# Optimization experiments

Measured on AMD Instinct MI355X. Metric: run time of the kernel, lower is better.

## Reference

```python
import jax, jax.numpy as jnp
import numpy as np

DIM = 768
FF = 3072
E = 8          # num_experts
K = 2          # top_k
H = 12         # n_heads
HD = DIM // H  # head dim
LN_EPS = 1e-5


def _layernorm(x, g, b):
    m = jnp.mean(x, axis=-1, keepdims=True)
    v = jnp.var(x, axis=-1, keepdims=True)
    return (x - m) * jax.lax.rsqrt(v + LN_EPS) * g + b


def _attention(x, Wqkv, Wproj):
    B, T, D = x.shape
    qkv = (x @ Wqkv).reshape(B, T, 3, H, HD)
    q, k, v = qkv[:, :, 0], qkv[:, :, 1], qkv[:, :, 2]  # [B,T,H,HD]
    scores = jnp.einsum('bqhd,bkhd->bhqk', q, k) * jnp.float32(HD) ** -0.5
    attn = jax.nn.softmax(scores, axis=-1)  # non-causal SDPA
    out = jnp.einsum('bhqk,bkhd->bqhd', attn, v).reshape(B, T, D)
    return out @ Wproj


def _moe(x, Wrouter, W1, W2):
    # world_size == 1 path of MoEFeedForward.forward:
    # gate_and_sort -> per-expert FFN -> weighted index_add unpermute.
    # Equivalent math: out[t] = sum_k softmax(topk_logits)[t,k] * expert_{idx[t,k]}(x[t]).
    B, T, D = x.shape
    xf = x.reshape(-1, D)                       # [N, D]
    N = xf.shape[0]
    logits = xf @ Wrouter                        # [N, E]
    topk_w, topk_idx = jax.lax.top_k(logits, K)  # [N, K]
    topk_w = jax.nn.softmax(topk_w.astype(jnp.float32), axis=-1).astype(x.dtype)
    # Combined per-expert weight for each token (sums duplicates, 0 if unrouted).
    we = jnp.zeros((N, E), x.dtype).at[jnp.arange(N)[:, None], topk_idx].add(topk_w)  # [N, E]

    def body(acc, expert):
        W1e, W2e, we_e = expert                 # [D,FF], [FF,D], [N]
        h = jax.nn.gelu(xf @ W1e, approximate=False)  # exact GELU like nn.GELU()
        return acc + we_e[:, None] * (h @ W2e), None

    out, _ = jax.lax.scan(body, jnp.zeros_like(xf), (W1, W2, we.T))
    return out.reshape(B, T, D)


def setup_inputs() -> dict:
    key = jax.random.key(0)
    ks = jax.random.split(key, 7)
    B, T = 4, 1024
    init = lambda k, shape, fan: jax.random.normal(k, shape, jnp.float32) * (fan ** -0.5)
    return {
        'x': jax.random.normal(ks[0], (B, T, DIM), jnp.float32),
        'Wqkv': init(ks[1], (DIM, 3 * DIM), DIM),
        'Wproj': init(ks[2], (DIM, DIM), DIM),
        'Wrouter': init(ks[3], (DIM, E), DIM),
        'W1': init(ks[4], (E, DIM, FF), DIM),
        'W2': init(ks[5], (E, FF, DIM), FF),
        'ln1_g': jnp.ones((DIM,), jnp.float32), 'ln1_b': jnp.zeros((DIM,), jnp.float32),
        'ln2_g': jnp.ones((DIM,), jnp.float32), 'ln2_b': jnp.zeros((DIM,), jnp.float32),
    }


def reference(x, Wqkv, Wproj, Wrouter, W1, W2, ln1_g, ln1_b, ln2_g, ln2_b):
    # PipelinedMoEBlock: pre-LN attention + pre-LN MoE FFN, residual connections.
    x = x + _attention(_layernorm(x, ln1_g, ln1_b), Wqkv, Wproj)
    x = x + _moe(_layernorm(x, ln2_g, ln2_b), Wrouter, W1, W2)
    return x
```

## Files before the change

### kernel.cpp

```cpp
#include <hip/hip_runtime.h>
#include <math.h>

typedef unsigned short u16;
typedef __attribute__((ext_vector_type(8))) short short8;
typedef __attribute__((ext_vector_type(4))) float f32x4;

#define DIMC   768
#define TOK    4096
#define NQKVC  2304
#define FFC    3072
#define NEXP   8
#define NHEAD  12
#define HDIM   64
#define SEQ    1024
#define NBATCH 4
#define SLOTS  9216

__device__ __forceinline__ float bf2f(u16 v) {
    unsigned int u = ((unsigned int)v) << 16;
    float f; __builtin_memcpy(&f, &u, 4); return f;
}
__device__ __forceinline__ u16 f2bf(float f) {
    unsigned int u; __builtin_memcpy(&u, &f, 4);
    u = (u + 0x7fffu + ((u >> 16) & 1u)) >> 16;
    return (u16)u;
}

__device__ __forceinline__ float fast_gelu(float v) {
    float x = fabsf(v) * 0.70710678118654752f;
    float t = __builtin_amdgcn_rcpf(1.f + 0.3275911f * x);
    float y = t * (0.254829592f + t * (-0.284496736f + t * (1.421413741f +
              t * (-1.453152027f + t * 1.061405429f))));
    float er = 1.f - y * __expf(-x * x);
    er = (v < 0.f) ? -er : er;
    return 0.5f * v * (1.f + er);
}

__device__ __forceinline__ void async16(u16* lds, const u16* gp) {
    __builtin_amdgcn_global_load_lds(
        (const __attribute__((address_space(1))) unsigned int*)gp,
        (__attribute__((address_space(3))) unsigned int*)lds, 16, 0, 0);
}

__global__ __launch_bounds__(256) void ln_split_kernel(const float* __restrict__ x,
                                                       const float* __restrict__ g,
                                                       const float* __restrict__ b,
                                                       u16* __restrict__ yh,
                                                       u16* __restrict__ yl) {
    int row = blockIdx.x, tid = threadIdx.x;
    const float* xr = x + (size_t)row * DIMC;
    float v[3];
#pragma unroll
    for (int i = 0; i < 3; i++) v[i] = xr[tid + 256 * i];
    float s = v[0] + v[1] + v[2];
    float q = v[0]*v[0] + v[1]*v[1] + v[2]*v[2];
#pragma unroll
    for (int o = 32; o; o >>= 1) { s += __shfl_down(s, o, 64); q += __shfl_down(q, o, 64); }
    __shared__ float rs[4], rq[4];
    if ((tid & 63) == 0) { rs[tid >> 6] = s; rq[tid >> 6] = q; }
    __syncthreads();
    s = rs[0] + rs[1] + rs[2] + rs[3];
    q = rq[0] + rq[1] + rq[2] + rq[3];
    float mean = s * (1.f / DIMC);
    float var  = q * (1.f / DIMC) - mean * mean;
    float rstd = rsqrtf(var + 1e-5f);
#pragma unroll
    for (int i = 0; i < 3; i++) {
        int c = tid + 256 * i;
        float o = (v[i] - mean) * rstd * g[c] + b[c];
        u16 h = f2bf(o);
        yh[(size_t)row * DIMC + c] = h;
        yl[(size_t)row * DIMC + c] = f2bf(o - bf2f(h));
    }
}

__global__ __launch_bounds__(256) void ln_bf_kernel(const float* __restrict__ x,
                                                    const float* __restrict__ g,
                                                    const float* __restrict__ b,
                                                    u16* __restrict__ yb,
                                                    float* __restrict__ yf) {
    int row = blockIdx.x, tid = threadIdx.x;
    const float* xr = x + (size_t)row * DIMC;
    float v[3];
#pragma unroll
    for (int i = 0; i < 3; i++) v[i] = xr[tid + 256 * i];
    float s = v[0] + v[1] + v[2];
    float q = v[0]*v[0] + v[1]*v[1] + v[2]*v[2];
#pragma unroll
    for (int o = 32; o; o >>= 1) { s += __shfl_down(s, o, 64); q += __shfl_down(q, o, 64); }
    __shared__ float rs[4], rq[4];
    if ((tid & 63) == 0) { rs[tid >> 6] = s; rq[tid >> 6] = q; }
    __syncthreads();
    s = rs[0] + rs[1] + rs[2] + rs[3];
    q = rq[0] + rq[1] + rq[2] + rq[3];
    float mean = s * (1.f / DIMC);
    float var  = q * (1.f / DIMC) - mean * mean;
    float rstd = rsqrtf(var + 1e-5f);
#pragma unroll
    for (int i = 0; i < 3; i++) {
        int c = tid + 256 * i;
        float o = (v[i] - mean) * rstd * g[c] + b[c];
        yb[(size_t)row * DIMC + c] = f2bf(o);
        yf[(size_t)row * DIMC + c] = o;
    }
}

__global__ __launch_bounds__(256) void split_hl_kernel(const float* __restrict__ src,
                                                       u16* __restrict__ dh,
                                                       u16* __restrict__ dl) {
    size_t i = ((size_t)blockIdx.x * 256 + threadIdx.x) * 4;
#pragma unroll
    for (int k = 0; k < 4; k++) {
        float v = src[i + k];
        u16 h = f2bf(v);
        dh[i + k] = h;
        dl[i + k] = f2bf(v - bf2f(h));
    }
}

__global__ __launch_bounds__(256) void transpose_split_kernel(
    const float* __restrict__ src, u16* __restrict__ dh, u16* __restrict__ dl,
    int s_rs, int d_rs, long s_bs, long d_bs) {
    __shared__ u16 th[32][33], tl[32][33];
    int z = blockIdx.z;
    const float* sb = src + (long)z * s_bs;
    int r0 = blockIdx.y * 32, c0 = blockIdx.x * 32;
    int tx = threadIdx.x & 31, ty = threadIdx.x >> 5;
#pragma unroll
    for (int i = 0; i < 4; i++) {
        float v = sb[(size_t)(r0 + ty + 8 * i) * s_rs + c0 + tx];
        u16 h = f2bf(v);
        th[ty + 8 * i][tx] = h;
        tl[ty + 8 * i][tx] = f2bf(v - bf2f(h));
    }
    __syncthreads();
#pragma unroll
    for (int i = 0; i < 4; i++) {
        size_t o = (long)z * d_bs + (size_t)(c0 + ty + 8 * i) * d_rs + r0 + tx;
        dh[o] = th[tx][ty + 8 * i];
        dl[o] = tl[tx][ty + 8 * i];
    }
}

__global__ __launch_bounds__(256) void transpose_f2b_kernel(
    const float* __restrict__ src, u16* __restrict__ dst,
    int s_rs, int d_rs, long s_bs, long d_bs) {
    __shared__ u16 tile[32][33];
    int z = blockIdx.z;
    const float* sb = src + (long)z * s_bs;
    int r0 = blockIdx.y * 32, c0 = blockIdx.x * 32;
    int tx = threadIdx.x & 31, ty = threadIdx.x >> 5;
#pragma unroll
    for (int i = 0; i < 4; i++)
        tile[ty + 8 * i][tx] = f2bf(sb[(size_t)(r0 + ty + 8 * i) * s_rs + c0 + tx]);
    __syncthreads();
#pragma unroll
    for (int i = 0; i < 4; i++)
        dst[(long)z * d_bs + (size_t)(c0 + ty + 8 * i) * d_rs + r0 + tx] = tile[tx][ty + 8 * i];
}

__global__ __launch_bounds__(256) void transpose_b2b_kernel(
    const u16* __restrict__ src, u16* __restrict__ dst,
    int s_rs, int d_rs, long s_bs1, int s_n1, long s_bs2, long d_bs) {
    __shared__ u16 tile[32][33];
    int z = blockIdx.z;
    const u16* sb = src + (long)(z / s_n1) * s_bs1 + (long)(z % s_n1) * s_bs2;
    u16* db = dst + (long)z * d_bs;
    int r0 = blockIdx.y * 32, c0 = blockIdx.x * 32;
    int tx = threadIdx.x & 31, ty = threadIdx.x >> 5;
#pragma unroll
    for (int i = 0; i < 4; i++)
        tile[ty + 8 * i][tx] = sb[(size_t)(r0 + ty + 8 * i) * s_rs + c0 + tx];
    __syncthreads();
#pragma unroll
    for (int i = 0; i < 4; i++)
        db[(size_t)(c0 + ty + 8 * i) * d_rs + r0 + tx] = tile[tx][ty + 8 * i];
}

template<int EPI, int OUT>
__global__ __launch_bounds__(256)
void gemm3_kernel(const u16* __restrict__ Ah, const u16* __restrict__ Al, int lda, long aBS,
                  const u16* __restrict__ Bh, const u16* __restrict__ Bl, int ldb, long bBS,
                  void* __restrict__ C0, void* __restrict__ C1, int ldc, long cBS,
                  int M, int N, int K, float alpha, const float* __restrict__ R) {
    __shared__ u16 Ash[128 * 32], Asl[128 * 32], Bsh[128 * 32], Bsl[128 * 32];
    int bm = blockIdx.y, bn = blockIdx.x, bz = blockIdx.z;
    int m0 = bm * 128, n0 = bn * 128;
    const u16* Ahb = Ah + (long)bz * aBS;
    const u16* Alb = Al + (long)bz * aBS;
    const u16* Bhb = Bh + (long)bz * bBS;
    const u16* Blb = Bl + (long)bz * bBS;
    int tid = threadIdx.x, wv = tid >> 6, ln = tid & 63;
    int quad = ln >> 4, l15 = ln & 15;
    int wm = wv & 1, wn = wv >> 1;
    f32x4 acc[4][4];
#pragma unroll
    for (int i = 0; i < 4; i++)
#pragma unroll
        for (int j = 0; j < 4; j++) acc[i][j] = (f32x4)0.f;
    int srow = ln >> 2, schk = (ln & 3) * 8;

    for (int k0 = 0; k0 < K; k0 += 32) {
#pragma unroll
        for (int j = 0; j < 2; j++) {
            int r = 32 * wv + 16 * j + srow;
            size_t ao = (size_t)(m0 + r) * lda + k0 + schk;
            async16(&Ash[(32 * wv + 16 * j) * 32], Ahb + ao);
            async16(&Asl[(32 * wv + 16 * j) * 32], Alb + ao);
            size_t bo = (size_t)(n0 + r) * ldb + k0 + schk;
            async16(&Bsh[(32 * wv + 16 * j) * 32], Bhb + bo);
            async16(&Bsl[(32 * wv + 16 * j) * 32], Blb + bo);
        }
        __syncthreads();
        short8 ah[4], al4[4], bh[4], bl4[4];
#pragma unroll
        for (int mi = 0; mi < 4; mi++) {
            int off = (64 * wm + 16 * mi + l15) * 32 + quad * 8;
            ah[mi]  = *(const short8*)&Ash[off];
            al4[mi] = *(const short8*)&Asl[off];
        }
#pragma unroll
        for (int ni = 0; ni < 4; ni++) {
            int off = (64 * wn + 16 * ni + l15) * 32 + quad * 8;
            bh[ni]  = *(const short8*)&Bsh[off];
            bl4[ni] = *(const short8*)&Bsl[off];
        }
#pragma unroll
        for (int mi = 0; mi < 4; mi++)
#pragma unroll
            for (int ni = 0; ni < 4; ni++) {
                acc[mi][ni] = __builtin_amdgcn_mfma_f32_16x16x32_bf16(ah[mi],  bh[ni],  acc[mi][ni], 0, 0, 0);
                acc[mi][ni] = __builtin_amdgcn_mfma_f32_16x16x32_bf16(ah[mi],  bl4[ni], acc[mi][ni], 0, 0, 0);
                acc[mi][ni] = __builtin_amdgcn_mfma_f32_16x16x32_bf16(al4[mi], bh[ni],  acc[mi][ni], 0, 0, 0);
            }
        __syncthreads();
    }
#pragma unroll
    for (int mi = 0; mi < 4; mi++) {
#pragma unroll
        for (int r = 0; r < 4; r++) {
            int row = m0 + 64 * wm + 16 * mi + quad * 4 + r;
#pragma unroll
            for (int ni = 0; ni < 4; ni++) {
                int col = n0 + 64 * wn + 16 * ni + l15;
                size_t idx = (long)bz * cBS + (size_t)row * ldc + col;
                float v = acc[mi][ni][r] * alpha;
                if (EPI == 3) v += R[idx];
                if (OUT == 1) ((float*)C0)[idx] = v;
                else {
                    u16 h = f2bf(v);
                    ((u16*)C0)[idx] = h;
                    ((u16*)C1)[idx] = f2bf(v - bf2f(h));
                }
            }
        }
    }
}

__global__ __launch_bounds__(256)
void gemm3_pv_kernel(const u16* __restrict__ Ph,
                     const u16* __restrict__ VTh_, const u16* __restrict__ VTl_,
                     float* __restrict__ attf, int b) {
    __shared__ u16 Ash[64 * 32], Asl[64 * 32], Bsh[64 * 32], Bsl[64 * 32];
    int kz = blockIdx.x, qt = blockIdx.y, h = blockIdx.z;
    int tid = threadIdx.x, wv = tid >> 6, ln = tid & 63;
    int quad = ln >> 4, l15 = ln & 15;
    const u16* Ah = Ph + (size_t)h * SEQ * 2 * SEQ;
    const u16* Al = Ah + SEQ;
    const u16* Bh = VTh_ + (size_t)h * HDIM * SEQ;
    const u16* Bl = VTl_ + (size_t)h * HDIM * SEQ;
    int m0 = qt * 64;
    f32x4 acc[4];
#pragma unroll
    for (int i = 0; i < 4; i++) acc[i] = (f32x4)0.f;
    int srow = ln >> 2, schk = (ln & 3) * 8;
    int kbase = kz * (SEQ / 4);
    for (int k0 = kbase; k0 < kbase + SEQ / 4; k0 += 32) {
        int r = 16 * wv + srow;
        async16(&Ash[(16 * wv) * 32], Ah + (size_t)(m0 + r) * 2 * SEQ + k0 + schk);
        async16(&Asl[(16 * wv) * 32], Al + (size_t)(m0 + r) * 2 * SEQ + k0 + schk);
        async16(&Bsh[(16 * wv) * 32], Bh + (size_t)r * SEQ + k0 + schk);
        async16(&Bsl[(16 * wv) * 32], Bl + (size_t)r * SEQ + k0 + schk);
        __syncthreads();
        short8 a_h = *(const short8*)&Ash[(16 * wv + l15) * 32 + quad * 8];
        short8 a_l = *(const short8*)&Asl[(16 * wv + l15) * 32 + quad * 8];
#pragma unroll
        for (int ni = 0; ni < 4; ni++) {
            short8 b_h = *(const short8*)&Bsh[(16 * ni + l15) * 32 + quad * 8];
            short8 b_l = *(const short8*)&Bsl[(16 * ni + l15) * 32 + quad * 8];
            acc[ni] = __builtin_amdgcn_mfma_f32_16x16x32_bf16(a_h, b_h, acc[ni], 0, 0, 0);
            acc[ni] = __builtin_amdgcn_mfma_f32_16x16x32_bf16(a_h, b_l, acc[ni], 0, 0, 0);
            acc[ni] = __builtin_amdgcn_mfma_f32_16x16x32_bf16(a_l, b_h, acc[ni], 0, 0, 0);
        }
        __syncthreads();
    }
#pragma unroll
    for (int ni = 0; ni < 4; ni++)
#pragma unroll
        for (int r = 0; r < 4; r++) {
            int q = m0 + 16 * wv + quad * 4 + r;
            int d = h * HDIM + 16 * ni + l15;
            atomicAdd(&attf[((size_t)b * SEQ + q) * DIMC + d], acc[ni][r]);
        }
}

template<int EPI, int OUTF>
__global__ __launch_bounds__(256)
void gemm_moe_kernel(const u16* __restrict__ A, int lda,
                     const u16* __restrict__ B, int ldb,
                     void* __restrict__ Cv, int ldc,
                     int N, int K,
                     const int* __restrict__ seg, long expStride) {
    __shared__ u16 As[128 * 32];
    __shared__ u16 Bs[128 * 32];
    int m0 = blockIdx.y * 128, n0 = blockIdx.x * 128;
    if (m0 >= seg[8]) return;
    int e = 0;
#pragma unroll
    for (int i = 1; i < 8; i++) if (m0 >= seg[i]) e = i;
    const u16* Bp = B + (long)e * expStride;
    int tid = threadIdx.x, wv = tid >> 6, ln = tid & 63;
    int quad = ln >> 4, l15 = ln & 15;
    int wm = wv & 1, wn = wv >> 1;
    f32x4 acc[4][4];
#pragma unroll
    for (int i = 0; i < 4; i++)
#pragma unroll
        for (int j = 0; j < 4; j++) acc[i][j] = (f32x4)0.f;
    int srow = ln >> 2, schk = (ln & 3) * 8;
    for (int k0 = 0; k0 < K; k0 += 32) {
#pragma unroll
        for (int j = 0; j < 2; j++) {
            int r = 32 * wv + 16 * j + srow;
            async16(&As[(32 * wv + 16 * j) * 32], A + (size_t)(m0 + r) * lda + k0 + schk);
            async16(&Bs[(32 * wv + 16 * j) * 32], Bp + (size_t)(n0 + r) * ldb + k0 + schk);
        }
        __syncthreads();
        short8 af[4], bfr[4];
#pragma unroll
        for (int mi = 0; mi < 4; mi++)
            af[mi] = *(const short8*)&As[(64 * wm + 16 * mi + l15) * 32 + quad * 8];
#pragma unroll
        for (int ni = 0; ni < 4; ni++)
            bfr[ni] = *(const short8*)&Bs[(64 * wn + 16 * ni + l15) * 32 + quad * 8];
#pragma unroll
        for (int mi = 0; mi < 4; mi++)
#pragma unroll
            for (int ni = 0; ni < 4; ni++)
                acc[mi][ni] = __builtin_amdgcn_mfma_f32_16x16x32_bf16(af[mi], bfr[ni], acc[mi][ni], 0, 0, 0);
        __syncthreads();
    }
#pragma unroll
    for (int mi = 0; mi < 4; mi++) {
#pragma unroll
        for (int r = 0; r < 4; r++) {
            int row = m0 + 64 * wm + 16 * mi + quad * 4 + r;
#pragma unroll
            for (int ni = 0; ni < 4; ni++) {
                int col = n0 + 64 * wn + 16 * ni + l15;
                float v = acc[mi][ni][r];
                if (EPI == 2) v = fast_gelu(v);
                size_t idx = (size_t)row * ldc + col;
                if (OUTF) ((float*)Cv)[idx] = v;
                else      ((u16*)Cv)[idx] = f2bf(v);
            }
        }
    }
}

__global__ __launch_bounds__(256)
void gemm_moe_n64_kernel(const u16* __restrict__ A, int lda,
                         const u16* __restrict__ B, int ldb,
                         float* __restrict__ C, int ldc,
                         int K, const int* __restrict__ seg, long expStride) {
    __shared__ u16 As[128 * 32];
    __shared__ u16 Bs[64 * 32];
    int m0 = blockIdx.y * 128, n0 = blockIdx.x * 64;
    if (m0 >= seg[8]) return;
    int e = 0;
#pragma unroll
    for (int i = 1; i < 8; i++) if (m0 >= seg[i]) e = i;
    const u16* Bp = B + (long)e * expStride;
    int tid = threadIdx.x, wv = tid >> 6, ln = tid & 63;
    int quad = ln >> 4, l15 = ln & 15;
    f32x4 acc[2][4];
#pragma unroll
    for (int i = 0; i < 2; i++)
#pragma unroll
        for (int j = 0; j < 4; j++) acc[i][j] = (f32x4)0.f;
    int srow = ln >> 2, schk = (ln & 3) * 8;
    for (int k0 = 0; k0 < K; k0 += 32) {
#pragma unroll
        for (int j = 0; j < 2; j++) {
            int r = 32 * wv + 16 * j + srow;
            async16(&As[(32 * wv + 16 * j) * 32], A + (size_t)(m0 + r) * lda + k0 + schk);
        }
        {
            int r = 16 * wv + srow;
            async16(&Bs[(16 * wv) * 32], Bp + (size_t)(n0 + r) * ldb + k0 + schk);
        }
        __syncthreads();
        short8 af[2], bfr[4];
#pragma unroll
        for (int mi = 0; mi < 2; mi++)
            af[mi] = *(const short8*)&As[(32 * wv + 16 * mi + l15) * 32 + quad * 8];
#pragma unroll
        for (int ni = 0; ni < 4; ni++)
            bfr[ni] = *(const short8*)&Bs[(16 * ni + l15) * 32 + quad * 8];
#pragma unroll
        for (int mi = 0; mi < 2; mi++)
#pragma unroll
            for (int ni = 0; ni < 4; ni++)
                acc[mi][ni] = __builtin_amdgcn_mfma_f32_16x16x32_bf16(af[mi], bfr[ni], acc[mi][ni], 0, 0, 0);
        __syncthreads();
    }
#pragma unroll
    for (int mi = 0; mi < 2; mi++)
#pragma unroll
        for (int r = 0; r < 4; r++) {
            int row = m0 + 32 * wv + 16 * mi + quad * 4 + r;
#pragma unroll
            for (int ni = 0; ni < 4; ni++) {
                int col = n0 + 16 * ni + l15;
                C[(size_t)row * ldc + col] = acc[mi][ni][r];
            }
        }
}

__global__ __launch_bounds__(256) void softmax_split_kernel(float* __restrict__ S) {
    size_t row = blockIdx.x;
    float* p = S + row * (size_t)SEQ;
    u16* ph = (u16*)p;
    u16* pl = (u16*)p + SEQ;
    int tid = threadIdx.x;
    float v[4];
#pragma unroll
    for (int i = 0; i < 4; i++) v[i] = p[tid + 256 * i];
    float m = fmaxf(fmaxf(v[0], v[1]), fmaxf(v[2], v[3]));
#pragma unroll
    for (int o = 32; o; o >>= 1) m = fmaxf(m, __shfl_down(m, o, 64));
    __shared__ float red[4], red2[4];
    if ((tid & 63) == 0) red[tid >> 6] = m;
    __syncthreads();
    m = fmaxf(fmaxf(red[0], red[1]), fmaxf(red[2], red[3]));
    float e[4], s = 0.f;
#pragma unroll
    for (int i = 0; i < 4; i++) { e[i] = expf(v[i] - m); s += e[i]; }
#pragma unroll
    for (int o = 32; o; o >>= 1) s += __shfl_down(s, o, 64);
    if ((tid & 63) == 0) red2[tid >> 6] = s;
    __syncthreads();
    s = red2[0] + red2[1] + red2[2] + red2[3];
    float inv = 1.f / s;
#pragma unroll
    for (int i = 0; i < 4; i++) {
        int c = tid + 256 * i;
        float w = e[i] * inv;
        u16 h = f2bf(w);
        ph[c] = h;
        pl[c] = f2bf(w - bf2f(h));
    }
}

__global__ __launch_bounds__(256) void router_kernel(const float* __restrict__ h2f,
                                                     const float* __restrict__ Wr,
                                                     int* __restrict__ topk_idx,
                                                     float* __restrict__ topk_w,
                                                     int* __restrict__ counts) {
    int t = blockIdx.x, tid = threadIdx.x;
    __shared__ float part[256 * 8];
    float l[8];
#pragma unroll
    for (int e = 0; e < 8; e++) l[e] = 0.f;
    const float* xr = h2f + (size_t)t * DIMC;
#pragma unroll
    for (int i = 0; i < 3; i++) {
        int c = tid + 256 * i;
        float xv = xr[c];
        const float* wr = Wr + (size_t)c * NEXP;
#pragma unroll
        for (int e = 0; e < 8; e++) l[e] += xv * wr[e];
    }
#pragma unroll
    for (int e = 0; e < 8; e++) part[tid * 8 + e] = l[e];
    for (int s = 128; s; s >>= 1) {
        __syncthreads();
        if (tid < s)
#pragma unroll
            for (int e = 0; e < 8; e++) part[tid * 8 + e] += part[(tid + s) * 8 + e];
    }
    __syncthreads();
    if (tid == 0) {
        float lg[8];
#pragma unroll
        for (int e = 0; e < 8; e++) lg[e] = part[e];
        int i0 = 0;
        for (int e = 1; e < 8; e++) if (lg[e] > lg[i0]) i0 = e;
        int i1 = -1;
        for (int e = 0; e < 8; e++) if (e != i0 && (i1 < 0 || lg[e] > lg[i1])) i1 = e;
        float w1 = expf(lg[i1] - lg[i0]);
        float den = 1.f + w1;
        topk_idx[2 * t] = i0; topk_idx[2 * t + 1] = i1;
        topk_w[2 * t] = 1.f / den;  topk_w[2 * t + 1] = w1 / den;
        atomicAdd(&counts[i0], 1); atomicAdd(&counts[i1], 1);
    }
}

__global__ void offsets_kernel(const int* __restrict__ counts,
                               int* __restrict__ seg, int* __restrict__ cursor) {
    if (threadIdx.x == 0 && blockIdx.x == 0) {
        int off = 0;
        for (int e = 0; e < 8; e++) {
            seg[e] = off; cursor[e] = off;
            off += ((counts[e] + 127) / 128) * 128;
        }
        seg[8] = off;
    }
}

__global__ __launch_bounds__(256) void build_perm_kernel(
    const int* __restrict__ topk_idx, const float* __restrict__ topk_w,
    int* __restrict__ cursor, int* __restrict__ perm,
    float* __restrict__ gatew, int* __restrict__ slot_of) {
    int t = blockIdx.x * 256 + threadIdx.x;
    if (t >= TOK) return;
#pragma unroll
    for (int j = 0; j < 2; j++) {
        int e = topk_idx[2 * t + j];
        int slot = atomicAdd(&cursor[e], 1);
        perm[slot] = t;
        gatew[slot] = topk_w[2 * t + j];
        slot_of[2 * t + j] = slot;
    }
}

__global__ __launch_bounds__(192) void gather_kernel(const u16* __restrict__ h2,
                                                     const int* __restrict__ perm,
                                                     u16* __restrict__ xg) {
    int slot = blockIdx.x;
    int t = perm[slot];
    const uint2* s = (const uint2*)(h2 + (size_t)t * DIMC);
    uint2* d = (uint2*)(xg + (size_t)slot * DIMC);
    d[threadIdx.x] = s[threadIdx.x];
}

__global__ __launch_bounds__(192) void combine_kernel(
    const float* __restrict__ x1, const float* __restrict__ yg,
    const float* __restrict__ gatew, const int* __restrict__ slot_of,
    float* __restrict__ out) {
    int t = blockIdx.x;
    int s0 = slot_of[2 * t], s1 = slot_of[2 * t + 1];
    float w0 = gatew[s0], w1 = gatew[s1];
    int c = threadIdx.x * 4;
    const float* xr = x1 + (size_t)t * DIMC;
    const float* y0 = yg + (size_t)s0 * DIMC;
    const float* y1 = yg + (size_t)s1 * DIMC;
    float* orow = out + (size_t)t * DIMC;
#pragma unroll
    for (int k = 0; k < 4; k++)
        orow[c + k] = xr[c + k] + w0 * y0[c + k] + w1 * y1[c + k];
}

extern "C" void kernel_launch(void* const* d_in, const int* in_sizes, int n_in,
                              void* d_out, int out_size, void* d_ws, size_t ws_size,
                              hipStream_t stream) {
    const float* x       = (const float*)d_in[0];
    const float* Wqkv    = (const float*)d_in[1];
    const float* Wproj   = (const float*)d_in[2];
    const float* Wrouter = (const float*)d_in[3];
    const float* W1      = (const float*)d_in[4];
    const float* W2      = (const float*)d_in[5];
    const float* ln1g    = (const float*)d_in[6];
    const float* ln1b    = (const float*)d_in[7];
    const float* ln2g    = (const float*)d_in[8];
    const float* ln2b    = (const float*)d_in[9];
    float* out = (float*)d_out;
    char* ws = (char*)d_ws;

    const size_t o_x1   = 0;
    const size_t o_rout = 12582912;
    const size_t P      = 12845056;
    const size_t WS_REQ = 177995776;
    if (ws_size < WS_REQ) return;

    float* x1 = (float*)(ws + o_x1);
    float* Sc    = (float*)(ws + P);
    u16*   qkvh  = (u16*)(ws + P + 50331648);
    u16*   qkvl  = (u16*)(ws + P + 69206016);
    u16*   VTh   = (u16*)(ws + P + 88080384);
    u16*   VTl   = (u16*)(ws + P + 94371840);
    u16*   atth  = (u16*)(ws + P + 100663296);
    u16*   attl  = (u16*)(ws + P + 106954752);
    u16*   h1h   = (u16*)(ws + P + 113246208);
    u16*   h1l   = (u16*)(ws + P + 119537664);
    float* attf  = (float*)(ws + P + 113246208);
    u16*   Wqh   = (u16*)(ws + P + 125829120);
    u16*   Wql   = (u16*)(ws + P + 129368064);
    u16*   Wph   = (u16*)(ws + P + 132907008);
    u16*   Wpl   = (u16*)(ws + P + 134086656);
    u16*   W1T   = (u16*)(ws + P);
    u16*   W2T   = (u16*)(ws + P + 37748736);
    u16*   h2    = (u16*)(ws + P + 75497472);
    float* h2f   = (float*)(ws + P + 81788928);
    u16*   xg    = (u16*)(ws + P + 94371840);
    u16*   hid   = (u16*)(ws + P + 108527616);
    float* yg    = (float*)(ws + P + 75497472);

    int*   counts   = (int*)(ws + o_rout + 0);
    int*   seg      = (int*)(ws + o_rout + 64);
    int*   cursor   = (int*)(ws + o_rout + 128);
    int*   topk_idx = (int*)(ws + o_rout + 1024);
    float* topk_w   = (float*)(ws + o_rout + 34816);
    int*   perm     = (int*)(ws + o_rout + 68608);
    float* gatew    = (float*)(ws + o_rout + 106496);
    int*   slot_of  = (int*)(ws + o_rout + 144384);

    const long EXPSTR = (long)DIMC * FFC;

    transpose_split_kernel<<<dim3(NQKVC/32, DIMC/32, 1), 256, 0, stream>>>(
        Wqkv, Wqh, Wql, NQKVC, DIMC, 0, 0);
    transpose_split_kernel<<<dim3(DIMC/32, DIMC/32, 1), 256, 0, stream>>>(
        Wproj, Wph, Wpl, DIMC, DIMC, 0, 0);
    ln_split_kernel<<<TOK, 256, 0, stream>>>(x, ln1g, ln1b, h1h, h1l);
    gemm3_kernel<0,2><<<dim3(NQKVC/128, TOK/128, 1), 256, 0, stream>>>(
        h1h, h1l, DIMC, 0, Wqh, Wql, DIMC, 0,
        qkvh, qkvl, NQKVC, 0, TOK, NQKVC, DIMC, 1.f, nullptr);
    (void)hipMemsetAsync(attf, 0, 12582912, stream);
    transpose_b2b_kernel<<<dim3(HDIM/32, SEQ/32, NBATCH*NHEAD), 256, 0, stream>>>(
        qkvh + 2 * DIMC, VTh, NQKVC, SEQ, (long)SEQ * NQKVC, NHEAD, (long)HDIM, (long)HDIM * SEQ);
    transpose_b2b_kernel<<<dim3(HDIM/32, SEQ/32, NBATCH*NHEAD), 256, 0, stream>>>(
        qkvl + 2 * DIMC, VTl, NQKVC, SEQ, (long)SEQ * NQKVC, NHEAD, (long)HDIM, (long)HDIM * SEQ);
    for (int b = 0; b < NBATCH; b++) {
        const u16* qbh = qkvh + (size_t)b * SEQ * NQKVC;
        const u16* qbl = qkvl + (size_t)b * SEQ * NQKVC;
        gemm3_kernel<0,1><<<dim3(SEQ/128, SEQ/128, NHEAD), 256, 0, stream>>>(
            qbh, qbl, NQKVC, (long)HDIM,
            qbh + DIMC, qbl + DIMC, NQKVC, (long)HDIM,
            Sc, nullptr, SEQ, (long)SEQ * SEQ,
            SEQ, SEQ, HDIM, 0.125f, nullptr);
        softmax_split_kernel<<<NHEAD * SEQ, 256, 0, stream>>>(Sc);
        gemm3_pv_kernel<<<dim3(4, SEQ/64, NHEAD), 256, 0, stream>>>(
            (const u16*)Sc,
            VTh + (size_t)b * NHEAD * HDIM * SEQ, VTl + (size_t)b * NHEAD * HDIM * SEQ,
            attf, b);
    }
    split_hl_kernel<<<(TOK * DIMC) / 1024, 256, 0, stream>>>(attf, atth, attl);
    gemm3_kernel<3,1><<<dim3(DIMC/128, TOK/128, 1), 256, 0, stream>>>(
        atth, attl, DIMC, 0, Wph, Wpl, DIMC, 0,
        x1, nullptr, DIMC, 0, TOK, DIMC, DIMC, 1.f, x);

    transpose_f2b_kernel<<<dim3(FFC/32, DIMC/32, NEXP), 256, 0, stream>>>(
        W1, W1T, FFC, DIMC, EXPSTR, EXPSTR);
    transpose_f2b_kernel<<<dim3(DIMC/32, FFC/32, NEXP), 256, 0, stream>>>(
        W2, W2T, DIMC, FFC, EXPSTR, EXPSTR);
    ln_bf_kernel<<<TOK, 256, 0, stream>>>(x1, ln2g, ln2b, h2, h2f);
    (void)hipMemsetAsync(ws + o_rout, 0, 262144, stream);
    router_kernel<<<TOK, 256, 0, stream>>>(h2f, Wrouter, topk_idx, topk_w, counts);
    offsets_kernel<<<1, 64, 0, stream>>>(counts, seg, cursor);
    build_perm_kernel<<<16, 256, 0, stream>>>(topk_idx, topk_w, cursor, perm, gatew, slot_of);
    gather_kernel<<<SLOTS, 192, 0, stream>>>(h2, perm, xg);
    gemm_moe_kernel<2,0><<<dim3(FFC/128, SLOTS/128, 1), 256, 0, stream>>>(
        xg, DIMC, W1T, DIMC, hid, FFC, FFC, DIMC, seg, EXPSTR);
    gemm_moe_n64_kernel<<<dim3(DIMC/64, SLOTS/128, 1), 256, 0, stream>>>(
        hid, FFC, W2T, FFC, yg, DIMC, FFC, seg, EXPSTR);
    combine_kernel<<<TOK, 192, 0, stream>>>(x1, yg, gatew, slot_of, out);

    (void)in_sizes; (void)n_in; (void)out_size;
}
```

Baseline: 888.8 us.

## Fuse softmax normalization into PV GEMM and deepen MoE GEMM K-tiles

The softmax kernel now only computes per-row max and reciprocal sum, and the PV kernel reads raw fp32 scores, exponentiates, normalizes and splits them into bf16 hi/lo inside the tile load. This removes the separate write and re-read of the split probability matrix. The MoE GEMMs are specialized to fixed shapes, process K in 64-wide steps with half as many barriers, and use a 1D grid remapped so consecutive blocks share expert weight tiles for better L2 reuse. The cost is exp work repeated in the PV kernel and larger shared-memory tiles.

```diff
diff --git a/kernel.cpp b/kernel.cpp
--- a/kernel.cpp
+++ b/kernel.cpp
@@ -257,33 +257,84 @@
     }
 }
 
+__global__ __launch_bounds__(256) void softmax_stats_kernel(const float* __restrict__ S,
+                                                            float* __restrict__ stats) {
+    size_t row = blockIdx.x;
+    const float* p = S + row * (size_t)SEQ;
+    int tid = threadIdx.x;
+    float v[4];
+#pragma unroll
+    for (int i = 0; i < 4; i++) v[i] = p[tid + 256 * i];
+    float m = fmaxf(fmaxf(v[0], v[1]), fmaxf(v[2], v[3]));
+#pragma unroll
+    for (int o = 32; o; o >>= 1) m = fmaxf(m, __shfl_down(m, o, 64));
+    __shared__ float red[4], red2[4];
+    if ((tid & 63) == 0) red[tid >> 6] = m;
+    __syncthreads();
+    m = fmaxf(fmaxf(red[0], red[1]), fmaxf(red[2], red[3]));
+    float s = 0.f;
+#pragma unroll
+    for (int i = 0; i < 4; i++) s += __expf(v[i] - m);
+#pragma unroll
+    for (int o = 32; o; o >>= 1) s += __shfl_down(s, o, 64);
+    if ((tid & 63) == 0) red2[tid >> 6] = s;
+    __syncthreads();
+    if (tid == 0) {
+        s = red2[0] + red2[1] + red2[2] + red2[3];
+        stats[row * 2]     = m;
+        stats[row * 2 + 1] = 1.f / s;
+    }
+}
+
 __global__ __launch_bounds__(256)
-void gemm3_pv_kernel(const u16* __restrict__ Ph,
+void pv_fused_kernel(const float* __restrict__ Sc, const float* __restrict__ stats,
                      const u16* __restrict__ VTh_, const u16* __restrict__ VTl_,
                      float* __restrict__ attf, int b) {
-    __shared__ u16 Ash[64 * 32], Asl[64 * 32], Bsh[64 * 32], Bsl[64 * 32];
+    __shared__ u16 Psh[64 * 32], Psl[64 * 32], Bsh[64 * 32], Bsl[64 * 32];
+    __shared__ float sm[64], sl[64];
     int kz = blockIdx.x, qt = blockIdx.y, h = blockIdx.z;
     int tid = threadIdx.x, wv = tid >> 6, ln = tid & 63;
     int quad = ln >> 4, l15 = ln & 15;
-    const u16* Ah = Ph + (size_t)h * SEQ * 2 * SEQ;
-    const u16* Al = Ah + SEQ;
+    int m0 = qt * 64;
+    const float* Sh = Sc + (size_t)h * SEQ * SEQ;
     const u16* Bh = VTh_ + (size_t)h * HDIM * SEQ;
     const u16* Bl = VTl_ + (size_t)h * HDIM * SEQ;
-    int m0 = qt * 64;
+    if (tid < 64) {
+        sm[tid] = stats[(h * SEQ + m0 + tid) * 2];
+        sl[tid] = stats[(h * SEQ + m0 + tid) * 2 + 1];
+    }
     f32x4 acc[4];
 #pragma unroll
     for (int i = 0; i < 4; i++) acc[i] = (f32x4)0.f;
+    int prow = tid >> 2;
+    int pk   = (tid & 3) * 8;
     int srow = ln >> 2, schk = (ln & 3) * 8;
     int kbase = kz * (SEQ / 4);
+    __syncthreads();
     for (int k0 = kbase; k0 < kbase + SEQ / 4; k0 += 32) {
-        int r = 16 * wv + srow;
-        async16(&Ash[(16 * wv) * 32], Ah + (size_t)(m0 + r) * 2 * SEQ + k0 + schk);
-        async16(&Asl[(16 * wv) * 32], Al + (size_t)(m0 + r) * 2 * SEQ + k0 + schk);
-        async16(&Bsh[(16 * wv) * 32], Bh + (size_t)r * SEQ + k0 + schk);
-        async16(&Bsl[(16 * wv) * 32], Bl + (size_t)r * SEQ + k0 + schk);
-        __syncthreads();
-        short8 a_h = *(const short8*)&Ash[(16 * wv + l15) * 32 + quad * 8];
-        short8 a_l = *(const short8*)&Asl[(16 * wv + l15) * 32 + quad * 8];
+        {
+            int r = 16 * wv + srow;
+            async16(&Bsh[(16 * wv) * 32], Bh + (size_t)r * SEQ + k0 + schk);
+            async16(&Bsl[(16 * wv) * 32], Bl + (size_t)r * SEQ + k0 + schk);
+        }
+        const float* sp = Sh + (size_t)(m0 + prow) * SEQ + k0 + pk;
+        float4 s0 = *(const float4*)sp;
+        float4 s1 = *(const float4*)(sp + 4);
+        float mr = sm[prow], lr = sl[prow];
+        float pv[8] = { s0.x, s0.y, s0.z, s0.w, s1.x, s1.y, s1.z, s1.w };
+        union { u16 u[8]; uint4 v; } ph, pl;
+#pragma unroll
+        for (int j = 0; j < 8; j++) {
+            float p = __expf(pv[j] - mr) * lr;
+            u16 hh = f2bf(p);
+            ph.u[j] = hh;
+            pl.u[j] = f2bf(p - bf2f(hh));
+        }
+        *(uint4*)&Psh[prow * 32 + pk] = ph.v;
+        *(uint4*)&Psl[prow * 32 + pk] = pl.v;
+        __syncthreads();
+        short8 a_h = *(const short8*)&Psh[(16 * wv + l15) * 32 + quad * 8];
+        short8 a_l = *(const short8*)&Psl[(16 * wv + l15) * 32 + quad * 8];
 #pragma unroll
         for (int ni = 0; ni < 4; ni++) {
             short8 b_h = *(const short8*)&Bsh[(16 * ni + l15) * 32 + quad * 8];
@@ -304,114 +355,126 @@
         }
 }
 
-template<int EPI, int OUTF>
 __global__ __launch_bounds__(256)
-void gemm_moe_kernel(const u16* __restrict__ A, int lda,
-                     const u16* __restrict__ B, int ldb,
-                     void* __restrict__ Cv, int ldc,
-                     int N, int K,
-                     const int* __restrict__ seg, long expStride) {
-    __shared__ u16 As[128 * 32];
-    __shared__ u16 Bs[128 * 32];
-    int m0 = blockIdx.y * 128, n0 = blockIdx.x * 128;
+void gemm1_kernel(const u16* __restrict__ A, const u16* __restrict__ B,
+                  u16* __restrict__ C, const int* __restrict__ seg) {
+    __shared__ u16 As[2 * 128 * 32];
+    __shared__ u16 Bs[2 * 128 * 32];
+    int i = blockIdx.x;
+    int mt = (i & 7) * 9 + ((i >> 3) % 9);
+    int nt = (i >> 3) / 9;
+    int m0 = mt * 128, n0 = nt * 128;
     if (m0 >= seg[8]) return;
     int e = 0;
 #pragma unroll
-    for (int i = 1; i < 8; i++) if (m0 >= seg[i]) e = i;
-    const u16* Bp = B + (long)e * expStride;
+    for (int j = 1; j < 8; j++) if (m0 >= seg[j]) e = j;
+    const u16* Bp = B + (long)e * DIMC * FFC;
     int tid = threadIdx.x, wv = tid >> 6, ln = tid & 63;
     int quad = ln >> 4, l15 = ln & 15;
     int wm = wv & 1, wn = wv >> 1;
     f32x4 acc[4][4];
 #pragma unroll
-    for (int i = 0; i < 4; i++)
-#pragma unroll
-        for (int j = 0; j < 4; j++) acc[i][j] = (f32x4)0.f;
+    for (int a = 0; a < 4; a++)
+#pragma unroll
+        for (int c = 0; c < 4; c++) acc[a][c] = (f32x4)0.f;
     int srow = ln >> 2, schk = (ln & 3) * 8;
-    for (int k0 = 0; k0 < K; k0 += 32) {
+    for (int k0 = 0; k0 < DIMC; k0 += 64) {
 #pragma unroll
         for (int j = 0; j < 2; j++) {
             int r = 32 * wv + 16 * j + srow;
-            async16(&As[(32 * wv + 16 * j) * 32], A + (size_t)(m0 + r) * lda + k0 + schk);
-            async16(&Bs[(32 * wv + 16 * j) * 32], Bp + (size_t)(n0 + r) * ldb + k0 + schk);
-        }
-        __syncthreads();
-        short8 af[4], bfr[4];
-#pragma unroll
-        for (int mi = 0; mi < 4; mi++)
-            af[mi] = *(const short8*)&As[(64 * wm + 16 * mi + l15) * 32 + quad * 8];
-#pragma unroll
-        for (int ni = 0; ni < 4; ni++)
-            bfr[ni] = *(const short8*)&Bs[(64 * wn + 16 * ni + l15) * 32 + quad * 8];
-#pragma unroll
-        for (int mi = 0; mi < 4; mi++)
+#pragma unroll
+            for (int kh = 0; kh < 2; kh++) {
+                async16(&As[kh * 4096 + (32 * wv + 16 * j) * 32],
+                        A + (size_t)(m0 + r) * DIMC + k0 + kh * 32 + schk);
+                async16(&Bs[kh * 4096 + (32 * wv + 16 * j) * 32],
+                        Bp + (size_t)(n0 + r) * DIMC + k0 + kh * 32 + schk);
+            }
+        }
+        __syncthreads();
+#pragma unroll
+        for (int kh = 0; kh < 2; kh++) {
+            short8 af[4], bfr[4];
+#pragma unroll
+            for (int mi = 0; mi < 4; mi++)
+                af[mi] = *(const short8*)&As[kh * 4096 + (64 * wm + 16 * mi + l15) * 32 + quad * 8];
 #pragma unroll
             for (int ni = 0; ni < 4; ni++)
-                acc[mi][ni] = __builtin_amdgcn_mfma_f32_16x16x32_bf16(af[mi], bfr[ni], acc[mi][ni], 0, 0, 0);
-        __syncthreads();
-    }
-#pragma unroll
-    for (int mi = 0; mi < 4; mi++) {
+                bfr[ni] = *(const short8*)&Bs[kh * 4096 + (64 * wn + 16 * ni + l15) * 32 + quad * 8];
+#pragma unroll
+            for (int mi = 0; mi < 4; mi++)
+#pragma unroll
+                for (int ni = 0; ni < 4; ni++)
+                    acc[mi][ni] = __builtin_amdgcn_mfma_f32_16x16x32_bf16(af[mi], bfr[ni], acc[mi][ni], 0, 0, 0);
+        }
+        __syncthreads();
+    }
+#pragma unroll
+    for (int mi = 0; mi < 4; mi++)
 #pragma unroll
         for (int r = 0; r < 4; r++) {
             int row = m0 + 64 * wm + 16 * mi + quad * 4 + r;
 #pragma unroll
             for (int ni = 0; ni < 4; ni++) {
                 int col = n0 + 64 * wn + 16 * ni + l15;
-                float v = acc[mi][ni][r];
-                if (EPI == 2) v = fast_gelu(v);
-                size_t idx = (size_t)row * ldc + col;
-                if (OUTF) ((float*)Cv)[idx] = v;
-                else      ((u16*)Cv)[idx] = f2bf(v);
+                C[(size_t)row * FFC + col] = f2bf(fast_gelu(acc[mi][ni][r]));
             }
         }
-    }
 }
 
 __global__ __launch_bounds__(256)
-void gemm_moe_n64_kernel(const u16* __restrict__ A, int lda,
-                         const u16* __restrict__ B, int ldb,
-                         float* __restrict__ C, int ldc,
-                         int K, const int* __restrict__ seg, long expStride) {
-    __shared__ u16 As[128 * 32];
-    __shared__ u16 Bs[64 * 32];
-    int m0 = blockIdx.y * 128, n0 = blockIdx.x * 64;
+void gemm2_kernel(const u16* __restrict__ A, const u16* __restrict__ B,
+                  float* __restrict__ C, const int* __restrict__ seg) {
+    __shared__ u16 As[2 * 128 * 32];
+    __shared__ u16 Bs[2 * 64 * 32];
+    int i = blockIdx.x;
+    int mt = (i & 7) * 9 + ((i >> 3) % 9);
+    int nt = (i >> 3) / 9;
+    int m0 = mt * 128, n0 = nt * 64;
     if (m0 >= seg[8]) return;
     int e = 0;
 #pragma unroll
-    for (int i = 1; i < 8; i++) if (m0 >= seg[i]) e = i;
-    const u16* Bp = B + (long)e * expStride;
+    for (int j = 1; j < 8; j++) if (m0 >= seg[j]) e = j;
+    const u16* Bp = B + (long)e * DIMC * FFC;
     int tid = threadIdx.x, wv = tid >> 6, ln = tid & 63;
     int quad = ln >> 4, l15 = ln & 15;
     f32x4 acc[2][4];
 #pragma unroll
-    for (int i = 0; i < 2; i++)
-#pragma unroll
-        for (int j = 0; j < 4; j++) acc[i][j] = (f32x4)0.f;
+    for (int a = 0; a < 2; a++)
+#pragma unroll
+        for (int c = 0; c < 4; c++) acc[a][c] = (f32x4)0.f;
     int srow = ln >> 2, schk = (ln & 3) * 8;
-    for (int k0 = 0; k0 < K; k0 += 32) {
+    for (int k0 = 0; k0 < FFC; k0 += 64) {
 #pragma unroll
         for (int j = 0; j < 2; j++) {
             int r = 32 * wv + 16 * j + srow;
-            async16(&As[(32 * wv + 16 * j) * 32], A + (size_t)(m0 + r) * lda + k0 + schk);
+#pragma unroll
+            for (int kh = 0; kh < 2; kh++)
+                async16(&As[kh * 4096 + (32 * wv + 16 * j) * 32],
+                        A + (size_t)(m0 + r) * FFC + k0 + kh * 32 + schk);
         }
         {
             int r = 16 * wv + srow;
-            async16(&Bs[(16 * wv) * 32], Bp + (size_t)(n0 + r) * ldb + k0 + schk);
-        }
-        __syncthreads();
-        short8 af[2], bfr[4];
-#pragma unroll
-        for (int mi = 0; mi < 2; mi++)
-            af[mi] = *(const short8*)&As[(32 * wv + 16 * mi + l15) * 32 + quad * 8];
-#pragma unroll
-        for (int ni = 0; ni < 4; ni++)
-            bfr[ni] = *(const short8*)&Bs[(16 * ni + l15) * 32 + quad * 8];
-#pragma unroll
-        for (int mi = 0; mi < 2; mi++)
+#pragma unroll
+            for (int kh = 0; kh < 2; kh++)
+                async16(&Bs[kh * 2048 + (16 * wv) * 32],
+                        Bp + (size_t)(n0 + r) * FFC + k0 + kh * 32 + schk);
+        }
+        __syncthreads();
+#pragma unroll
+        for (int kh = 0; kh < 2; kh++) {
+            short8 af[2], bfr[4];
+#pragma unroll
+            for (int mi = 0; mi < 2; mi++)
+                af[mi] = *(const short8*)&As[kh * 4096 + (32 * wv + 16 * mi + l15) * 32 + quad * 8];
 #pragma unroll
             for (int ni = 0; ni < 4; ni++)
-                acc[mi][ni] = __builtin_amdgcn_mfma_f32_16x16x32_bf16(af[mi], bfr[ni], acc[mi][ni], 0, 0, 0);
+                bfr[ni] = *(const short8*)&Bs[kh * 2048 + (16 * ni + l15) * 32 + quad * 8];
+#pragma unroll
+            for (int mi = 0; mi < 2; mi++)
+#pragma unroll
+                for (int ni = 0; ni < 4; ni++)
+                    acc[mi][ni] = __builtin_amdgcn_mfma_f32_16x16x32_bf16(af[mi], bfr[ni], acc[mi][ni], 0, 0, 0);
+        }
         __syncthreads();
     }
 #pragma unroll
@@ -422,44 +485,9 @@
 #pragma unroll
             for (int ni = 0; ni < 4; ni++) {
                 int col = n0 + 16 * ni + l15;
-                C[(size_t)row * ldc + col] = acc[mi][ni][r];
+                C[(size_t)row * DIMC + col] = acc[mi][ni][r];
             }
         }
-}
-
-__global__ __launch_bounds__(256) void softmax_split_kernel(float* __restrict__ S) {
-    size_t row = blockIdx.x;
-    float* p = S + row * (size_t)SEQ;
-    u16* ph = (u16*)p;
-    u16* pl = (u16*)p + SEQ;
-    int tid = threadIdx.x;
-    float v[4];
-#pragma unroll
-    for (int i = 0; i < 4; i++) v[i] = p[tid + 256 * i];
-    float m = fmaxf(fmaxf(v[0], v[1]), fmaxf(v[2], v[3]));
-#pragma unroll
-    for (int o = 32; o; o >>= 1) m = fmaxf(m, __shfl_down(m, o, 64));
-    __shared__ float red[4], red2[4];
-    if ((tid & 63) == 0) red[tid >> 6] = m;
-    __syncthreads();
-    m = fmaxf(fmaxf(red[0], red[1]), fmaxf(red[2], red[3]));
-    float e[4], s = 0.f;
-#pragma unroll
-    for (int i = 0; i < 4; i++) { e[i] = expf(v[i] - m); s += e[i]; }
-#pragma unroll
-    for (int o = 32; o; o >>= 1) s += __shfl_down(s, o, 64);
-    if ((tid & 63) == 0) red2[tid >> 6] = s;
-    __syncthreads();
-    s = red2[0] + red2[1] + red2[2] + red2[3];
-    float inv = 1.f / s;
-#pragma unroll
-    for (int i = 0; i < 4; i++) {
-        int c = tid + 256 * i;
-        float w = e[i] * inv;
-        u16 h = f2bf(w);
-        ph[c] = h;
-        pl[c] = f2bf(w - bf2f(h));
-    }
 }
 
 __global__ __launch_bounds__(256) void router_kernel(const float* __restrict__ h2f,
@@ -598,6 +626,7 @@
     u16*   Wql   = (u16*)(ws + P + 129368064);
     u16*   Wph   = (u16*)(ws + P + 132907008);
     u16*   Wpl   = (u16*)(ws + P + 134086656);
+    float* stats = (float*)(ws + P + 135266304);
     u16*   W1T   = (u16*)(ws + P);
     u16*   W2T   = (u16*)(ws + P + 37748736);
     u16*   h2    = (u16*)(ws + P + 75497472);
@@ -638,9 +667,9 @@
             qbh + DIMC, qbl + DIMC, NQKVC, (long)HDIM,
             Sc, nullptr, SEQ, (long)SEQ * SEQ,
             SEQ, SEQ, HDIM, 0.125f, nullptr);
-        softmax_split_kernel<<<NHEAD * SEQ, 256, 0, stream>>>(Sc);
-        gemm3_pv_kernel<<<dim3(4, SEQ/64, NHEAD), 256, 0, stream>>>(
-            (const u16*)Sc,
+        softmax_stats_kernel<<<NHEAD * SEQ, 256, 0, stream>>>(Sc, stats);
+        pv_fused_kernel<<<dim3(4, SEQ/64, NHEAD), 256, 0, stream>>>(
+            Sc, stats,
             VTh + (size_t)b * NHEAD * HDIM * SEQ, VTl + (size_t)b * NHEAD * HDIM * SEQ,
             attf, b);
     }
@@ -659,10 +688,8 @@
     offsets_kernel<<<1, 64, 0, stream>>>(counts, seg, cursor);
     build_perm_kernel<<<16, 256, 0, stream>>>(topk_idx, topk_w, cursor, perm, gatew, slot_of);
     gather_kernel<<<SLOTS, 192, 0, stream>>>(h2, perm, xg);
-    gemm_moe_kernel<2,0><<<dim3(FFC/128, SLOTS/128, 1), 256, 0, stream>>>(
-        xg, DIMC, W1T, DIMC, hid, FFC, FFC, DIMC, seg, EXPSTR);
-    gemm_moe_n64_kernel<<<dim3(DIMC/64, SLOTS/128, 1), 256, 0, stream>>>(
-        hid, FFC, W2T, FFC, yg, DIMC, FFC, seg, EXPSTR);
+    gemm1_kernel<<<1728, 256, 0, stream>>>(xg, W1T, hid, seg);
+    gemm2_kernel<<<864, 256, 0, stream>>>(hid, W2T, yg, seg);
     combine_kernel<<<TOK, 192, 0, stream>>>(x1, yg, gatew, slot_of, out);
 
     (void)in_sizes; (void)n_in; (void)out_size;
```

Result: faster. 827.2 us (-6.9%).
